# Kernel optimization log

Measured on AMD Instinct MI355X. Metric: run time of the kernel, lower is better.

The kernel has to match this reference:

```python
import jax, jax.numpy as jnp
import numpy as np

N_NODES = 100000
N_EDGES = 6400000
D = 12

def setup_inputs() -> dict:
    key = jax.random.key(0)
    k1, k2, k3, k4 = jax.random.split(key, 4)
    x = jax.random.normal(k1, (N_NODES, D), dtype=jnp.float32)
    W_l = jax.random.normal(k2, (D, D), dtype=jnp.float32) / np.sqrt(D)
    W_r = jax.random.normal(k3, (D, D), dtype=jnp.float32) / np.sqrt(D)
    b = jnp.zeros((D,), dtype=jnp.float32)
    edge_index = jax.random.randint(k4, (2, N_EDGES), 0, N_NODES, dtype=jnp.int64)
    return {"x": x, "W_l": W_l, "W_r": W_r, "b": b, "edge_index": edge_index}

def reference(x, W_l, W_r, b, edge_index):
    # PyG SAGEConv (mean aggregation): out = lin_l(mean_{j in N(i)} x_j) + lin_r(x_i)
    src = edge_index[0]
    dst = edge_index[1]
    n = x.shape[0]
    msgs = x[src]                                      # [E, D] gather
    agg = jax.ops.segment_sum(msgs, dst, num_segments=n)          # [N, D]
    cnt = jax.ops.segment_sum(jnp.ones_like(dst, dtype=x.dtype), dst, num_segments=n)
    mean = agg / jnp.maximum(cnt, 1.0)[:, None]        # [N, D]
    out = mean @ W_l.T + x @ W_r.T + b                 # lin_l carries the bias in PyG
    return out
```

## Files before the change

kernel.cpp:

```cpp
#include <hip/hip_runtime.h>

#define N_NODES 100000
#define N_EDGES 6400000
#define D 12

#define SLOG 5
#define SSZ  32
#define NB   ((N_NODES + SSZ - 1) / SSZ)
#define NBLK 512
#define EPB  ((N_EDGES + NBLK - 1) / NBLK)
#define RSTR 13

#define CAP  1280
#define EPT  (CAP / 256)

__device__ __forceinline__ unsigned int f2bf(float f) {
    unsigned int u = __float_as_uint(f);
    return (u + 0x7fffu + ((u >> 16) & 1u)) >> 16;
}
__device__ __forceinline__ unsigned int pk2(float lo, float hi) {
    return (f2bf(hi) << 16) | f2bf(lo);
}
__device__ __forceinline__ float bflo(unsigned int u) { return __uint_as_float(u << 16); }
__device__ __forceinline__ float bfhi(unsigned int u) { return __uint_as_float(u & 0xffff0000u); }

__global__ __launch_bounds__(256) void prep_kernel(
    const float* __restrict__ x, unsigned int* __restrict__ xb)
{
    int i = blockIdx.x * 256 + threadIdx.x;
    if (i >= N_NODES) return;
    const float4* xr = (const float4*)(x) + (size_t)i * 3;
    float4 a = xr[0], b = xr[1], c = xr[2];
    unsigned int* o = xb + (size_t)i * 8;
    ((uint4*)o)[0] = make_uint4(pk2(a.x, a.y), pk2(a.z, a.w), pk2(b.x, b.y), pk2(b.z, b.w));
    ((uint2*)(o + 4))[0] = make_uint2(pk2(c.x, c.y), pk2(c.z, c.w));
}

__global__ __launch_bounds__(256) void hist_kernel(
    const int* __restrict__ ei, int* __restrict__ bins)
{
    __shared__ int h[NB];
    for (int i = threadIdx.x; i < NB; i += 256) h[i] = 0;
    __syncthreads();
    const int* dei = ei + N_EDGES;
    int start = blockIdx.x * EPB;
    int end = min(start + EPB, N_EDGES);
    int e = start + (int)threadIdx.x;
    while (e + 768 < end) {
        int d0 = dei[e], d1 = dei[e + 256], d2 = dei[e + 512], d3 = dei[e + 768];
        atomicAdd(&h[d0 >> SLOG], 1);
        atomicAdd(&h[d1 >> SLOG], 1);
        atomicAdd(&h[d2 >> SLOG], 1);
        atomicAdd(&h[d3 >> SLOG], 1);
        e += 1024;
    }
    while (e < end) { atomicAdd(&h[dei[e] >> SLOG], 1); e += 256; }
    __syncthreads();
    for (int i = threadIdx.x; i < NB; i += 256) {
        int c = h[i];
        if (c) atomicAdd(&bins[i], c);
    }
}

__global__ __launch_bounds__(1024) void scan_kernel(
    const int* __restrict__ bins, int* __restrict__ base, int* __restrict__ cursor)
{
    __shared__ int buf[1024];
    __shared__ int carry;
    int tid = threadIdx.x;
    if (tid == 0) carry = 0;
    __syncthreads();
    for (int c0 = 0; c0 < NB; c0 += 1024) {
        int i = c0 + tid;
        int v = (i < NB) ? bins[i] : 0;
        buf[tid] = v;
        __syncthreads();
        for (int o = 1; o < 1024; o <<= 1) {
            int t = (tid >= o) ? buf[tid - o] : 0;
            __syncthreads();
            buf[tid] += t;
            __syncthreads();
        }
        int excl = buf[tid] - v + carry;
        if (i < NB) { base[i] = excl; cursor[i] = excl; }
        __syncthreads();
        if (tid == 0) carry += buf[1023];
        __syncthreads();
    }
    if (tid == 0) base[NB] = N_EDGES;
}

__global__ __launch_bounds__(256) void scatter_sort_kernel(
    const int* __restrict__ ei, int* __restrict__ cursor,
    unsigned int* __restrict__ sorted)
{
    __shared__ int h[NB];
    for (int i = threadIdx.x; i < NB; i += 256) h[i] = 0;
    __syncthreads();
    const int* dei = ei + N_EDGES;
    int start = blockIdx.x * EPB;
    int end = min(start + EPB, N_EDGES);
    int e = start + (int)threadIdx.x;
    while (e + 768 < end) {
        int d0 = dei[e], d1 = dei[e + 256], d2 = dei[e + 512], d3 = dei[e + 768];
        atomicAdd(&h[d0 >> SLOG], 1);
        atomicAdd(&h[d1 >> SLOG], 1);
        atomicAdd(&h[d2 >> SLOG], 1);
        atomicAdd(&h[d3 >> SLOG], 1);
        e += 1024;
    }
    while (e < end) { atomicAdd(&h[dei[e] >> SLOG], 1); e += 256; }
    __syncthreads();
    for (int i = threadIdx.x; i < NB; i += 256) {
        int c = h[i];
        h[i] = c ? atomicAdd(&cursor[i], c) : 0;
    }
    __syncthreads();
    e = start + (int)threadIdx.x;
    while (e + 768 < end) {
        int s0 = ei[e], s1 = ei[e + 256], s2 = ei[e + 512], s3 = ei[e + 768];
        int d0 = dei[e], d1 = dei[e + 256], d2 = dei[e + 512], d3 = dei[e + 768];
        int p0 = atomicAdd(&h[d0 >> SLOG], 1);
        int p1 = atomicAdd(&h[d1 >> SLOG], 1);
        int p2 = atomicAdd(&h[d2 >> SLOG], 1);
        int p3 = atomicAdd(&h[d3 >> SLOG], 1);
        sorted[p0] = ((unsigned)s0 << SLOG) | (unsigned)(d0 & (SSZ - 1));
        sorted[p1] = ((unsigned)s1 << SLOG) | (unsigned)(d1 & (SSZ - 1));
        sorted[p2] = ((unsigned)s2 << SLOG) | (unsigned)(d2 & (SSZ - 1));
        sorted[p3] = ((unsigned)s3 << SLOG) | (unsigned)(d3 & (SSZ - 1));
        e += 1024;
    }
    while (e < end) {
        int s = ei[e], d = dei[e];
        int pos = atomicAdd(&h[d >> SLOG], 1);
        sorted[pos] = ((unsigned)s << SLOG) | (unsigned)(d & (SSZ - 1));
        e += 256;
    }
}

__global__ __launch_bounds__(256, 4) void agg_finalize_kernel(
    const unsigned int* __restrict__ sorted, const int* __restrict__ base,
    const unsigned int* __restrict__ xb,
    const float* __restrict__ x, const float* __restrict__ Wl,
    const float* __restrict__ Wr, const float* __restrict__ bias,
    float* __restrict__ out)
{
    __shared__ float sWl[D * D], sWr[D * D], sb[D];
    __shared__ int cnt[SSZ];
    __shared__ int segbase[SSZ + 1];
    __shared__ int cursor[SSZ];
    __shared__ int cnt_tot[SSZ];
    __shared__ unsigned vals[CAP * 6];

    int t = threadIdx.x;
    int b = blockIdx.x;

    if (t < D * D) { sWl[t] = Wl[t]; sWr[t] = Wr[t]; }
    if (t < D) sb[t] = bias[t];
    if (t < SSZ) cnt_tot[t] = 0;

    float acc[D];
#pragma unroll
    for (int d = 0; d < D; ++d) acc[d] = 0.f;

    int loc = t >> 3;
    int sub = t & 7;

    int start = base[b];
    int end = base[b + 1];

    for (int c0 = start; c0 < end; c0 += CAP) {
        int n = min(CAP, end - c0);
        if (t < SSZ) cnt[t] = 0;
        __syncthreads();

        unsigned pe[EPT];
        int ne = 0;
        for (int j = t; j < n; j += 256) pe[ne++] = sorted[c0 + j];
#pragma unroll
        for (int k = 0; k < EPT; ++k)
            if (k < ne) atomicAdd(&cnt[pe[k] & (SSZ - 1)], 1);
        __syncthreads();

        if (t == 0) {
            int s = 0;
#pragma unroll
            for (int i = 0; i < SSZ; ++i) { segbase[i] = s; s += cnt[i]; }
            segbase[SSZ] = s;
        }
        __syncthreads();
        if (t < SSZ) { cursor[t] = segbase[t]; cnt_tot[t] += cnt[t]; }
        __syncthreads();

#pragma unroll
        for (int k = 0; k < EPT; ++k) {
            if (k < ne) {
                unsigned p = pe[k];
                int slot = atomicAdd(&cursor[p & (SSZ - 1)], 1);
                const unsigned* r = xb + (size_t)(p >> SLOG) * 8;
                uint2 q0 = ((const uint2*)r)[0];
                uint2 q1 = ((const uint2*)r)[1];
                uint2 q2 = ((const uint2*)r)[2];
                unsigned* vv = &vals[slot * 6];
                ((uint2*)vv)[0] = q0;
                ((uint2*)vv)[1] = q1;
                ((uint2*)vv)[2] = q2;
            }
        }
        __syncthreads();

        int s0 = segbase[loc], s1 = segbase[loc + 1];
        for (int j = s0 + sub; j < s1; j += 8) {
            const unsigned* vv = &vals[j * 6];
            uint2 q0 = ((const uint2*)vv)[0];
            uint2 q1 = ((const uint2*)vv)[1];
            uint2 q2 = ((const uint2*)vv)[2];
            acc[0]  += bflo(q0.x); acc[1]  += bfhi(q0.x);
            acc[2]  += bflo(q0.y); acc[3]  += bfhi(q0.y);
            acc[4]  += bflo(q1.x); acc[5]  += bfhi(q1.x);
            acc[6]  += bflo(q1.y); acc[7]  += bfhi(q1.y);
            acc[8]  += bflo(q2.x); acc[9]  += bfhi(q2.x);
            acc[10] += bflo(q2.y); acc[11] += bfhi(q2.y);
        }
        __syncthreads();
    }

    float* red = (float*)vals;
#pragma unroll
    for (int d = 0; d < D; ++d) red[sub * 417 + loc * 13 + d] = acc[d];
    __syncthreads();

    if (t < SSZ) {
        int node = b * SSZ + t;
        float m[D];
#pragma unroll
        for (int d = 0; d < D; ++d) {
            float s = 0.f;
#pragma unroll
            for (int ss = 0; ss < 8; ++ss) s += red[ss * 417 + t * 13 + d];
            m[d] = s;
        }
        float inv = 1.f / fmaxf((float)cnt_tot[t], 1.f);
#pragma unroll
        for (int d = 0; d < D; ++d) m[d] *= inv;

        float xi[D];
        const float4* xr = (const float4*)(x) + (size_t)node * 3;
        float4 x0 = xr[0], x1 = xr[1], x2 = xr[2];
        xi[0] = x0.x; xi[1] = x0.y; xi[2]  = x0.z; xi[3]  = x0.w;
        xi[4] = x1.x; xi[5] = x1.y; xi[6]  = x1.z; xi[7]  = x1.w;
        xi[8] = x2.x; xi[9] = x2.y; xi[10] = x2.z; xi[11] = x2.w;

        float o[D];
#pragma unroll
        for (int oo = 0; oo < D; ++oo) {
            float a = sb[oo];
#pragma unroll
            for (int d = 0; d < D; ++d) {
                a += m[d] * sWl[oo * D + d];
                a += xi[d] * sWr[oo * D + d];
            }
            o[oo] = a;
        }
        float4* orow = (float4*)(out) + (size_t)node * 3;
        orow[0] = make_float4(o[0], o[1], o[2], o[3]);
        orow[1] = make_float4(o[4], o[5], o[6], o[7]);
        orow[2] = make_float4(o[8], o[9], o[10], o[11]);
    }
}

__global__ __launch_bounds__(256) void agg_finalize_f32_kernel(
    const unsigned int* __restrict__ sorted, const int* __restrict__ base,
    const float* __restrict__ x, const float* __restrict__ Wl,
    const float* __restrict__ Wr, const float* __restrict__ bias,
    float* __restrict__ out)
{
    __shared__ float agg[SSZ * RSTR];
    __shared__ float sWl[D * D], sWr[D * D], sb[D];
    int t = threadIdx.x;
    int b = blockIdx.x;
    for (int i = t; i < SSZ * RSTR; i += 256) agg[i] = 0.f;
    if (t < D * D) { sWl[t] = Wl[t]; sWr[t] = Wr[t]; }
    if (t < D) sb[t] = bias[t];
    __syncthreads();
    int start = base[b];
    int end = base[b + 1];
    for (int e = start + t; e < end; e += 256) {
        unsigned p = sorted[e];
        int src = (int)(p >> SLOG);
        int lc = (int)(p & (SSZ - 1));
        const float4* xr = (const float4*)(x) + (size_t)src * 3;
        float4 a = xr[0], b4 = xr[1], c = xr[2];
        float* ar = &agg[lc * RSTR];
        atomicAdd(ar + 0,  a.x);  atomicAdd(ar + 1,  a.y);
        atomicAdd(ar + 2,  a.z);  atomicAdd(ar + 3,  a.w);
        atomicAdd(ar + 4,  b4.x); atomicAdd(ar + 5,  b4.y);
        atomicAdd(ar + 6,  b4.z); atomicAdd(ar + 7,  b4.w);
        atomicAdd(ar + 8,  c.x);  atomicAdd(ar + 9,  c.y);
        atomicAdd(ar + 10, c.z);  atomicAdd(ar + 11, c.w);
        atomicAdd(ar + 12, 1.f);
    }
    __syncthreads();
    if (t < SSZ) {
        int node = b * SSZ + t;
        const float* ar = &agg[t * RSTR];
        float inv = 1.f / fmaxf(ar[12], 1.f);
        float m[D], xi[D];
#pragma unroll
        for (int d = 0; d < D; ++d) m[d] = ar[d] * inv;
        const float4* xr = (const float4*)(x) + (size_t)node * 3;
        float4 x0 = xr[0], x1 = xr[1], x2 = xr[2];
        xi[0] = x0.x; xi[1] = x0.y; xi[2]  = x0.z; xi[3]  = x0.w;
        xi[4] = x1.x; xi[5] = x1.y; xi[6]  = x1.z; xi[7]  = x1.w;
        xi[8] = x2.x; xi[9] = x2.y; xi[10] = x2.z; xi[11] = x2.w;
        float o[D];
#pragma unroll
        for (int oo = 0; oo < D; ++oo) {
            float a = sb[oo];
#pragma unroll
            for (int d = 0; d < D; ++d) {
                a += m[d] * sWl[oo * D + d];
                a += xi[d] * sWr[oo * D + d];
            }
            o[oo] = a;
        }
        float4* orow = (float4*)(out) + (size_t)node * 3;
        orow[0] = make_float4(o[0], o[1], o[2], o[3]);
        orow[1] = make_float4(o[4], o[5], o[6], o[7]);
        orow[2] = make_float4(o[8], o[9], o[10], o[11]);
    }
}


__global__ __launch_bounds__(256) void scatter_kernel(
    const int* __restrict__ ei, const float* __restrict__ x,
    float* __restrict__ agg, float* __restrict__ cnt)
{
    int e = blockIdx.x * blockDim.x + threadIdx.x;
    if (e >= N_EDGES) return;
    int src = ei[e];
    int dst = ei[N_EDGES + e];
    const float4* xr = (const float4*)(x + (size_t)src * D);
    float4 a = xr[0], b4 = xr[1], c = xr[2];
    float* dr = agg + (size_t)dst * D;
    atomicAdd(dr + 0,  a.x);  atomicAdd(dr + 1,  a.y);
    atomicAdd(dr + 2,  a.z);  atomicAdd(dr + 3,  a.w);
    atomicAdd(dr + 4,  b4.x); atomicAdd(dr + 5,  b4.y);
    atomicAdd(dr + 6,  b4.z); atomicAdd(dr + 7,  b4.w);
    atomicAdd(dr + 8,  c.x);  atomicAdd(dr + 9,  c.y);
    atomicAdd(dr + 10, c.z);  atomicAdd(dr + 11, c.w);
    atomicAdd(cnt + dst, 1.0f);
}

__global__ __launch_bounds__(256) void finalize_kernel(
    const float* __restrict__ x, const float* __restrict__ Wl,
    const float* __restrict__ Wr, const float* __restrict__ bias,
    const float* __restrict__ agg, const float* __restrict__ cnt,
    float* __restrict__ out)
{
    __shared__ float sWl[D * D], sWr[D * D], sb[D];
    int t = threadIdx.x;
    if (t < D * D) { sWl[t] = Wl[t]; sWr[t] = Wr[t]; }
    if (t < D) sb[t] = bias[t];
    __syncthreads();
    int i = blockIdx.x * blockDim.x + t;
    if (i >= N_NODES) return;
    float inv = 1.0f / fmaxf(cnt[i], 1.0f);
    float m[D], xi[D];
    const float4* ar = (const float4*)(agg + (size_t)i * D);
    const float4* xr = (const float4*)(x + (size_t)i * D);
    float4 a0 = ar[0], a1 = ar[1], a2 = ar[2];
    float4 x0 = xr[0], x1 = xr[1], x2 = xr[2];
    m[0] = a0.x * inv; m[1] = a0.y * inv; m[2]  = a0.z * inv; m[3]  = a0.w * inv;
    m[4] = a1.x * inv; m[5] = a1.y * inv; m[6]  = a1.z * inv; m[7]  = a1.w * inv;
    m[8] = a2.x * inv; m[9] = a2.y * inv; m[10] = a2.z * inv; m[11] = a2.w * inv;
    xi[0] = x0.x; xi[1] = x0.y; xi[2]  = x0.z; xi[3]  = x0.w;
    xi[4] = x1.x; xi[5] = x1.y; xi[6]  = x1.z; xi[7]  = x1.w;
    xi[8] = x2.x; xi[9] = x2.y; xi[10] = x2.z; xi[11] = x2.w;
    float o[D];
#pragma unroll
    for (int oo = 0; oo < D; ++oo) {
        float acc = sb[oo];
#pragma unroll
        for (int d = 0; d < D; ++d) {
            acc += m[d] * sWl[oo * D + d];
            acc += xi[d] * sWr[oo * D + d];
        }
        o[oo] = acc;
    }
    float4* orow = (float4*)(out + (size_t)i * D);
    orow[0] = make_float4(o[0], o[1], o[2], o[3]);
    orow[1] = make_float4(o[4], o[5], o[6], o[7]);
    orow[2] = make_float4(o[8], o[9], o[10], o[11]);
}

extern "C" void kernel_launch(void* const* d_in, const int* in_sizes, int n_in,
                              void* d_out, int out_size, void* d_ws, size_t ws_size,
                              hipStream_t stream) {
    const float* x    = (const float*)d_in[0];
    const float* Wl   = (const float*)d_in[1];
    const float* Wr   = (const float*)d_in[2];
    const float* bias = (const float*)d_in[3];
    const int*   ei   = (const int*)d_in[4];
    float* out = (float*)d_out;

    size_t sortedBytes = (size_t)N_EDGES * sizeof(unsigned int);
    size_t xbBytes     = (size_t)N_NODES * 8 * sizeof(unsigned int);
    size_t binsBytes   = (size_t)NB * sizeof(int);
    size_t baseBytes   = (size_t)(NB + 1) * sizeof(int);
    size_t neededFull = sortedBytes + xbBytes + binsBytes + baseBytes + binsBytes;
    size_t neededMid  = sortedBytes + binsBytes + baseBytes + binsBytes;

    if (ws_size >= neededFull) {
        char* p = (char*)d_ws;
        unsigned int* sorted = (unsigned int*)p;        p += sortedBytes;
        unsigned int* xb     = (unsigned int*)p;        p += xbBytes;
        int* bins   = (int*)p;                          p += binsBytes;
        int* base   = (int*)p;                          p += baseBytes;
        int* cursor = (int*)p;

        hipMemsetAsync(bins, 0, binsBytes, stream);
        prep_kernel<<<(N_NODES + 255) / 256, 256, 0, stream>>>(x, xb);
        hist_kernel<<<NBLK, 256, 0, stream>>>(ei, bins);
        scan_kernel<<<1, 1024, 0, stream>>>(bins, base, cursor);
        scatter_sort_kernel<<<NBLK, 256, 0, stream>>>(ei, cursor, sorted);
        agg_finalize_kernel<<<NB, 256, 0, stream>>>(sorted, base, xb, x, Wl, Wr, bias, out);
    } else if (ws_size >= neededMid) {
        char* p = (char*)d_ws;
        unsigned int* sorted = (unsigned int*)p;        p += sortedBytes;
        int* bins   = (int*)p;                          p += binsBytes;
        int* base   = (int*)p;                          p += baseBytes;
        int* cursor = (int*)p;

        hipMemsetAsync(bins, 0, binsBytes, stream);
        hist_kernel<<<NBLK, 256, 0, stream>>>(ei, bins);
        scan_kernel<<<1, 1024, 0, stream>>>(bins, base, cursor);
        scatter_sort_kernel<<<NBLK, 256, 0, stream>>>(ei, cursor, sorted);
        agg_finalize_f32_kernel<<<NB, 256, 0, stream>>>(sorted, base, x, Wl, Wr, bias, out);
    } else {
        float* agg = (float*)d_ws;
        float* cnt = agg + (size_t)N_NODES * D;
        hipMemsetAsync(d_ws, 0, ((size_t)N_NODES * D + N_NODES) * sizeof(float), stream);
        scatter_kernel<<<(N_EDGES + 255) / 256, 256, 0, stream>>>(ei, x, agg, cnt);
        finalize_kernel<<<(N_NODES + 255) / 256, 256, 0, stream>>>(x, Wl, Wr, bias, agg, cnt, out);
    }
}
```

Measured before the change: 304.8 us.

## Widen node buckets to 128, prefetch gathers, parallel scan, padded LDS stride

Raises the per-block destination bucket from 32 to 128 nodes, so there are fewer, larger blocks and a smaller bucket index in the packed sort key. The bf16 row gathers are issued right after the edge loads, before the counting atomics and barriers, so global latency overlaps the shared-memory histogram. The serial prefix sum on thread 0 becomes a wavefront shuffle scan, and the LDS value stride is padded from 6 to 7 words to reduce bank conflicts. Each node is now reduced by only 2 threads instead of 8, which gives less parallelism per node and uses more registers for the prefetched rows. Bounds checks are added because 100000 is not a multiple of 128.

```diff
diff --git a/kernel.cpp b/kernel.cpp
--- a/kernel.cpp
+++ b/kernel.cpp
@@ -4,8 +4,8 @@
 #define N_EDGES 6400000
 #define D 12
 
-#define SLOG 5
-#define SSZ  32
+#define SLOG 7
+#define SSZ  128
 #define NB   ((N_NODES + SSZ - 1) / SSZ)
 #define NBLK 512
 #define EPB  ((N_EDGES + NBLK - 1) / NBLK)
@@ -13,6 +13,8 @@
 
 #define CAP  1280
 #define EPT  (CAP / 256)
+#define VSTR 7
+#define REDS (SSZ * 13 + 5)
 
 __device__ __forceinline__ unsigned int f2bf(float f) {
     unsigned int u = __float_as_uint(f);
@@ -150,10 +152,12 @@
     __shared__ int segbase[SSZ + 1];
     __shared__ int cursor[SSZ];
     __shared__ int cnt_tot[SSZ];
-    __shared__ unsigned vals[CAP * 6];
+    __shared__ int wsum0;
+    __shared__ unsigned vals[CAP * VSTR];
 
     int t = threadIdx.x;
     int b = blockIdx.x;
+    int lane = t & 63;
 
     if (t < D * D) { sWl[t] = Wl[t]; sWr[t] = Wr[t]; }
     if (t < D) sb[t] = bias[t];
@@ -163,8 +167,8 @@
 #pragma unroll
     for (int d = 0; d < D; ++d) acc[d] = 0.f;
 
-    int loc = t >> 3;
-    int sub = t & 7;
+    int loc = t >> 1;
+    int sub = t & 1;
 
     int start = base[b];
     int end = base[b + 1];
@@ -177,17 +181,32 @@
         unsigned pe[EPT];
         int ne = 0;
         for (int j = t; j < n; j += 256) pe[ne++] = sorted[c0 + j];
+        uint2 q[EPT][3];
+#pragma unroll
+        for (int k = 0; k < EPT; ++k) {
+            if (k < ne) {
+                const unsigned* r = xb + (size_t)(pe[k] >> SLOG) * 8;
+                q[k][0] = ((const uint2*)r)[0];
+                q[k][1] = ((const uint2*)r)[1];
+                q[k][2] = ((const uint2*)r)[2];
+            }
+        }
 #pragma unroll
         for (int k = 0; k < EPT; ++k)
             if (k < ne) atomicAdd(&cnt[pe[k] & (SSZ - 1)], 1);
         __syncthreads();
 
-        if (t == 0) {
-            int s = 0;
-#pragma unroll
-            for (int i = 0; i < SSZ; ++i) { segbase[i] = s; s += cnt[i]; }
-            segbase[SSZ] = s;
-        }
+        int v = (t < SSZ) ? cnt[t] : 0;
+#pragma unroll
+        for (int o = 1; o < 64; o <<= 1) {
+            int u = __shfl_up(v, o);
+            if (lane >= o) v += u;
+        }
+        if (t == 63) wsum0 = v;
+        __syncthreads();
+        int incl = v + ((t >= 64 && t < SSZ) ? wsum0 : 0);
+        if (t < SSZ) segbase[t + 1] = incl;
+        if (t == 0) segbase[0] = 0;
         __syncthreads();
         if (t < SSZ) { cursor[t] = segbase[t]; cnt_tot[t] += cnt[t]; }
         __syncthreads();
@@ -195,23 +214,18 @@
 #pragma unroll
         for (int k = 0; k < EPT; ++k) {
             if (k < ne) {
-                unsigned p = pe[k];
-                int slot = atomicAdd(&cursor[p & (SSZ - 1)], 1);
-                const unsigned* r = xb + (size_t)(p >> SLOG) * 8;
-                uint2 q0 = ((const uint2*)r)[0];
-                uint2 q1 = ((const uint2*)r)[1];
-                uint2 q2 = ((const uint2*)r)[2];
-                unsigned* vv = &vals[slot * 6];
-                ((uint2*)vv)[0] = q0;
-                ((uint2*)vv)[1] = q1;
-                ((uint2*)vv)[2] = q2;
+                int slot = atomicAdd(&cursor[pe[k] & (SSZ - 1)], 1);
+                unsigned* vv = &vals[slot * VSTR];
+                ((uint2*)vv)[0] = q[k][0];
+                ((uint2*)vv)[1] = q[k][1];
+                ((uint2*)vv)[2] = q[k][2];
             }
         }
         __syncthreads();
 
         int s0 = segbase[loc], s1 = segbase[loc + 1];
-        for (int j = s0 + sub; j < s1; j += 8) {
-            const unsigned* vv = &vals[j * 6];
+        for (int j = s0 + sub; j < s1; j += 2) {
+            const unsigned* vv = &vals[j * VSTR];
             uint2 q0 = ((const uint2*)vv)[0];
             uint2 q1 = ((const uint2*)vv)[1];
             uint2 q2 = ((const uint2*)vv)[2];
@@ -227,45 +241,43 @@
 
     float* red = (float*)vals;
 #pragma unroll
-    for (int d = 0; d < D; ++d) red[sub * 417 + loc * 13 + d] = acc[d];
+    for (int d = 0; d < D; ++d) red[sub * REDS + loc * 13 + d] = acc[d];
     __syncthreads();
 
     if (t < SSZ) {
         int node = b * SSZ + t;
-        float m[D];
-#pragma unroll
-        for (int d = 0; d < D; ++d) {
-            float s = 0.f;
-#pragma unroll
-            for (int ss = 0; ss < 8; ++ss) s += red[ss * 417 + t * 13 + d];
-            m[d] = s;
-        }
-        float inv = 1.f / fmaxf((float)cnt_tot[t], 1.f);
-#pragma unroll
-        for (int d = 0; d < D; ++d) m[d] *= inv;
-
-        float xi[D];
-        const float4* xr = (const float4*)(x) + (size_t)node * 3;
-        float4 x0 = xr[0], x1 = xr[1], x2 = xr[2];
-        xi[0] = x0.x; xi[1] = x0.y; xi[2]  = x0.z; xi[3]  = x0.w;
-        xi[4] = x1.x; xi[5] = x1.y; xi[6]  = x1.z; xi[7]  = x1.w;
-        xi[8] = x2.x; xi[9] = x2.y; xi[10] = x2.z; xi[11] = x2.w;
-
-        float o[D];
-#pragma unroll
-        for (int oo = 0; oo < D; ++oo) {
-            float a = sb[oo];
-#pragma unroll
-            for (int d = 0; d < D; ++d) {
-                a += m[d] * sWl[oo * D + d];
-                a += xi[d] * sWr[oo * D + d];
+        if (node < N_NODES) {
+            float m[D];
+#pragma unroll
+            for (int d = 0; d < D; ++d)
+                m[d] = red[t * 13 + d] + red[REDS + t * 13 + d];
+            float inv = 1.f / fmaxf((float)cnt_tot[t], 1.f);
+#pragma unroll
+            for (int d = 0; d < D; ++d) m[d] *= inv;
+
+            float xi[D];
+            const float4* xr = (const float4*)(x) + (size_t)node * 3;
+            float4 x0 = xr[0], x1 = xr[1], x2 = xr[2];
+            xi[0] = x0.x; xi[1] = x0.y; xi[2]  = x0.z; xi[3]  = x0.w;
+            xi[4] = x1.x; xi[5] = x1.y; xi[6]  = x1.z; xi[7]  = x1.w;
+            xi[8] = x2.x; xi[9] = x2.y; xi[10] = x2.z; xi[11] = x2.w;
+
+            float o[D];
+#pragma unroll
+            for (int oo = 0; oo < D; ++oo) {
+                float a = sb[oo];
+#pragma unroll
+                for (int d = 0; d < D; ++d) {
+                    a += m[d] * sWl[oo * D + d];
+                    a += xi[d] * sWr[oo * D + d];
+                }
+                o[oo] = a;
             }
-            o[oo] = a;
-        }
-        float4* orow = (float4*)(out) + (size_t)node * 3;
-        orow[0] = make_float4(o[0], o[1], o[2], o[3]);
-        orow[1] = make_float4(o[4], o[5], o[6], o[7]);
-        orow[2] = make_float4(o[8], o[9], o[10], o[11]);
+            float4* orow = (float4*)(out) + (size_t)node * 3;
+            orow[0] = make_float4(o[0], o[1], o[2], o[3]);
+            orow[1] = make_float4(o[4], o[5], o[6], o[7]);
+            orow[2] = make_float4(o[8], o[9], o[10], o[11]);
+        }
     }
 }
 
@@ -303,31 +315,33 @@
     __syncthreads();
     if (t < SSZ) {
         int node = b * SSZ + t;
-        const float* ar = &agg[t * RSTR];
-        float inv = 1.f / fmaxf(ar[12], 1.f);
-        float m[D], xi[D];
-#pragma unroll
-        for (int d = 0; d < D; ++d) m[d] = ar[d] * inv;
-        const float4* xr = (const float4*)(x) + (size_t)node * 3;
-        float4 x0 = xr[0], x1 = xr[1], x2 = xr[2];
-        xi[0] = x0.x; xi[1] = x0.y; xi[2]  = x0.z; xi[3]  = x0.w;
-        xi[4] = x1.x; xi[5] = x1.y; xi[6]  = x1.z; xi[7]  = x1.w;
-        xi[8] = x2.x; xi[9] = x2.y; xi[10] = x2.z; xi[11] = x2.w;
-        float o[D];
-#pragma unroll
-        for (int oo = 0; oo < D; ++oo) {
-            float a = sb[oo];
-#pragma unroll
-            for (int d = 0; d < D; ++d) {
-                a += m[d] * sWl[oo * D + d];
-                a += xi[d] * sWr[oo * D + d];
+        if (node < N_NODES) {
+            const float* ar = &agg[t * RSTR];
+            float inv = 1.f / fmaxf(ar[12], 1.f);
+            float m[D], xi[D];
+#pragma unroll
+            for (int d = 0; d < D; ++d) m[d] = ar[d] * inv;
+            const float4* xr = (const float4*)(x) + (size_t)node * 3;
+            float4 x0 = xr[0], x1 = xr[1], x2 = xr[2];
+            xi[0] = x0.x; xi[1] = x0.y; xi[2]  = x0.z; xi[3]  = x0.w;
+            xi[4] = x1.x; xi[5] = x1.y; xi[6]  = x1.z; xi[7]  = x1.w;
+            xi[8] = x2.x; xi[9] = x2.y; xi[10] = x2.z; xi[11] = x2.w;
+            float o[D];
+#pragma unroll
+            for (int oo = 0; oo < D; ++oo) {
+                float a = sb[oo];
+#pragma unroll
+                for (int d = 0; d < D; ++d) {
+                    a += m[d] * sWl[oo * D + d];
+                    a += xi[d] * sWr[oo * D + d];
+                }
+                o[oo] = a;
             }
-            o[oo] = a;
-        }
-        float4* orow = (float4*)(out) + (size_t)node * 3;
-        orow[0] = make_float4(o[0], o[1], o[2], o[3]);
-        orow[1] = make_float4(o[4], o[5], o[6], o[7]);
-        orow[2] = make_float4(o[8], o[9], o[10], o[11]);
+            float4* orow = (float4*)(out) + (size_t)node * 3;
+            orow[0] = make_float4(o[0], o[1], o[2], o[3]);
+            orow[1] = make_float4(o[4], o[5], o[6], o[7]);
+            orow[2] = make_float4(o[8], o[9], o[10], o[11]);
+        }
     }
 }
 
```

Result: slower. 323.9 us (+6.3%).
